# Kernel tuning notes

Hardware: AMD Instinct MI355X
Metric: run time of the kernel (lower is better)

## Reference

```python
import jax, jax.numpy as jnp
import numpy as np

THETA = 10000.0

def apply_rope(x, token_positions, theta=THETA):
    # x: (..., seq, d_k); token_positions: (seq,)
    d_k = x.shape[-1]
    freqs = 1.0 / theta ** (jnp.arange(0, d_k, 2, dtype=jnp.float32) / d_k)  # (d_k/2,)
    ang = token_positions.astype(jnp.float32)[:, None] * freqs  # (seq, d_k/2)
    cos, sin = jnp.cos(ang), jnp.sin(ang)
    x_even, x_odd = x[..., 0::2], x[..., 1::2]
    out_even = x_even * cos - x_odd * sin
    out_odd = x_even * sin + x_odd * cos
    out = jnp.stack([out_even, out_odd], axis=-1)  # interleave pairs
    return out.reshape(*x.shape[:-1], d_k)


def setup_inputs() -> dict:
    key = jax.random.key(0)
    ks = jax.random.split(key, 5)
    B, S, D = 1, 4096, 1024
    s = 1.0 / np.sqrt(D)
    return {
        "x": jax.random.normal(ks[0], (B, S, D), dtype=jnp.float32),
        "token_positions": jnp.arange(S, dtype=jnp.int64 if jax.config.jax_enable_x64 else jnp.int32),
        "Wq": jax.random.normal(ks[1], (D, D), dtype=jnp.float32) * s,
        "Wk": jax.random.normal(ks[2], (D, D), dtype=jnp.float32) * s,
        "Wv": jax.random.normal(ks[3], (D, D), dtype=jnp.float32) * s,
        "Wo": jax.random.normal(ks[4], (D, D), dtype=jnp.float32) * s,
    }


def reference(x, token_positions, Wq, Wk, Wv, Wo):
    B, S, D = x.shape
    H = 16
    hd = D // H
    # nn.Linear(bias=False): y = x @ W.T
    q = (x @ Wq.T).reshape(B, S, H, hd).transpose(0, 2, 1, 3)  # (B,H,S,hd)
    k = (x @ Wk.T).reshape(B, S, H, hd).transpose(0, 2, 1, 3)
    v = (x @ Wv.T).reshape(B, S, H, hd).transpose(0, 2, 1, 3)
    q = apply_rope(q, token_positions)
    k = apply_rope(k, token_positions)
    scores = jnp.einsum("bhqd,bhkd->bhqk", q, k) / jnp.sqrt(jnp.float32(hd))
    causal = jnp.triu(jnp.ones((S, S), dtype=bool), k=1)  # True above diagonal
    scores = jnp.where(causal[None, None], -jnp.inf, scores)
    attn = jax.nn.softmax(scores, axis=-1)
    out = jnp.einsum("bhqk,bhkd->bhqd", attn, v)  # (B,H,S,hd)
    out = out.transpose(0, 2, 1, 3).reshape(B, S, D)
    return out @ Wo.T
```

## Files before the change

### kernel.cpp

```cpp
#include <hip/hip_runtime.h>
#include <hip/hip_bf16.h>
#include <math.h>

#define S_LEN 4096
#define D_MODEL 1024
#define NHEAD 16
#define HD 64

typedef short bf16x8 __attribute__((ext_vector_type(8)));
typedef float f32x16 __attribute__((ext_vector_type(16)));
typedef _Float16 f16x8 __attribute__((ext_vector_type(8)));
typedef _Float16 f16x4 __attribute__((ext_vector_type(4)));

static __device__ __forceinline__ unsigned pk2(float lo, float hi) {
  __hip_bfloat162 h = __float22bfloat162_rn(make_float2(lo, hi));
  return *reinterpret_cast<unsigned*>(&h);
}

static __device__ __forceinline__ void gload16(const void* g, void* l) {
  __builtin_amdgcn_global_load_lds(
      (const __attribute__((address_space(1))) unsigned*)g,
      (__attribute__((address_space(3))) unsigned*)l, 16, 0, 0);
}

__global__ __launch_bounds__(256)
void cvt_f16(const float* __restrict__ src, _Float16* __restrict__ dst, int n4) {
  for (int i = blockIdx.x * 256 + threadIdx.x; i < n4; i += gridDim.x * 256) {
    float4 v = ((const float4*)src)[i];
    f16x4 o;
    o[0] = (_Float16)v.x; o[1] = (_Float16)v.y;
    o[2] = (_Float16)v.z; o[3] = (_Float16)v.w;
    ((f16x4*)dst)[i] = o;
  }
}

__global__ __launch_bounds__(256)
void cvt4_f16(const float* __restrict__ s0, const float* __restrict__ s1,
              const float* __restrict__ s2, const float* __restrict__ s3,
              _Float16* __restrict__ d0, _Float16* __restrict__ d1,
              _Float16* __restrict__ d2, _Float16* __restrict__ d3, int n4) {
  const float* s = (blockIdx.y == 0) ? s0 : (blockIdx.y == 1) ? s1
                 : (blockIdx.y == 2) ? s2 : s3;
  _Float16* d = (blockIdx.y == 0) ? d0 : (blockIdx.y == 1) ? d1
              : (blockIdx.y == 2) ? d2 : d3;
  for (int i = blockIdx.x * 256 + threadIdx.x; i < n4; i += gridDim.x * 256) {
    float4 v = ((const float4*)s)[i];
    f16x4 o;
    o[0] = (_Float16)v.x; o[1] = (_Float16)v.y;
    o[2] = (_Float16)v.z; o[3] = (_Float16)v.w;
    ((f16x4*)d)[i] = o;
  }
}

#define BUFBYTES 16384

static __device__ __forceinline__ void gemm_mainloop_f16(
    const _Float16* __restrict__ A, const _Float16* __restrict__ B,
    int tr0, int br0, char* ldsbuf, int tid,
    f32x16& acc00, f32x16& acc01, f32x16& acc10, f32x16& acc11) {
  const int lane = tid & 63, w = tid >> 6;
  const int l31 = lane & 31, hi5 = lane >> 5;
  const int wr = (w >> 1) * 64, wc = (w & 1) * 64;

  const _Float16* srcs[4];
  int offs[4];
#pragma unroll
  for (int j = 0; j < 4; ++j) {
    int ch = w + 4 * j;
    if (ch < 8) {
      int u = ch * 64 + lane;
      srcs[j] = A + (size_t)(tr0 + (u & 127)) * 1024 + (u >> 7) * 8;
      offs[j] = ch * 1024;
    } else {
      int u = (ch - 8) * 64 + lane;
      srcs[j] = B + (size_t)(br0 + (u & 127)) * 1024 + (u >> 7) * 8;
      offs[j] = 8192 + (ch - 8) * 1024;
    }
  }

#define STAGE(bufoff, koff)                                           \
  {                                                                   \
    _Pragma("unroll") for (int j = 0; j < 4; ++j)                     \
        gload16(srcs[j] + (koff), ldsbuf + (bufoff) + offs[j]);       \
  }

#define COMPUTE(bufoff)                                               \
  {                                                                   \
    const char* lb = ldsbuf + (bufoff);                               \
    _Pragma("unroll") for (int s = 0; s < 2; ++s) {                   \
      const int c = 2 * s + hi5;                                      \
      const char* pa = lb + (size_t)(c * 128 + wr + l31) * 16;        \
      f16x8 a0 = *(const f16x8*)(pa);                                 \
      f16x8 a1 = *(const f16x8*)(pa + 512);                           \
      const char* pb = lb + 8192 + (size_t)(c * 128 + wc + l31) * 16; \
      f16x8 b0 = *(const f16x8*)(pb);                                 \
      f16x8 b1 = *(const f16x8*)(pb + 512);                           \
      acc00 = __builtin_amdgcn_mfma_f32_32x32x16_f16(a0, b0, acc00, 0, 0, 0); \
      acc01 = __builtin_amdgcn_mfma_f32_32x32x16_f16(a0, b1, acc01, 0, 0, 0); \
      acc10 = __builtin_amdgcn_mfma_f32_32x32x16_f16(a1, b0, acc10, 0, 0, 0); \
      acc11 = __builtin_amdgcn_mfma_f32_32x32x16_f16(a1, b1, acc11, 0, 0, 0); \
    }                                                                 \
  }

  STAGE(0, 0);
  __syncthreads();

#pragma unroll 1
  for (int it = 0; it < 16; ++it) {
    const int t0 = 2 * it;
    if (t0 < 31) STAGE(BUFBYTES, (t0 + 1) * 32);
    COMPUTE(0);
    __syncthreads();
    if (t0 + 1 < 31) STAGE(0, (t0 + 2) * 32);
    COMPUTE(BUFBYTES);
    __syncthreads();
  }
#undef STAGE
#undef COMPUTE
}

__global__ __launch_bounds__(256)
void qkv_gemm(const _Float16* __restrict__ xf,
              const _Float16* __restrict__ wqf, const _Float16* __restrict__ wkf,
              const _Float16* __restrict__ wvf,
              unsigned short* __restrict__ Qo, unsigned short* __restrict__ Ko,
              unsigned short* __restrict__ Vo, const int* __restrict__ pos) {
  __shared__ __align__(16) char ldsbuf[2 * BUFBYTES];
  const int tid = threadIdx.x;
  const int nb = blockIdx.x;
  const int which = nb >> 3;
  const int br0 = (nb & 7) * 128;
  const int tr0 = blockIdx.y * 128;

  const _Float16* Bsrc = (which == 0) ? wqf : (which == 1) ? wkf : wvf;
  unsigned short* Out = (which == 0) ? Qo : (which == 1) ? Ko : Vo;

  f32x16 acc00, acc01, acc10, acc11;
#pragma unroll
  for (int r = 0; r < 16; ++r) {
    acc00[r] = 0.0f; acc01[r] = 0.0f; acc10[r] = 0.0f; acc11[r] = 0.0f;
  }

  gemm_mainloop_f16(xf, Bsrc, tr0, br0, ldsbuf, tid, acc00, acc01, acc10, acc11);

  const int lane = tid & 63, w = tid >> 6;
  const int l31 = lane & 31, hi5 = lane >> 5;
  const int wr = (w >> 1) * 64, wc = (w & 1) * 64;
  const float qs = (which == 0) ? 0.125f : 1.0f;

#pragma unroll
  for (int bc = 0; bc < 2; ++bc) {
    const int n = br0 + wc + bc * 32 + l31;
    const int ch = n & 63;
    const float fr = 1.0f / powf(10000.0f, (float)(ch & ~1) * (1.0f / 64.0f));
#pragma unroll
    for (int ar = 0; ar < 2; ++ar) {
      const f32x16& a = ar ? (bc ? acc11 : acc10) : (bc ? acc01 : acc00);
#pragma unroll
      for (int r = 0; r < 16; ++r) {
        const int m = tr0 + wr + ar * 32 + (r & 3) + 8 * (r >> 2) + 4 * hi5;
        float v = a[r];
        if (which < 2) {
          const float ang = (float)pos[m] * fr;
          float sn, cs;
          __sincosf(ang, &sn, &cs);
          const float vp = __shfl_xor(v, 1);
          v = (ch & 1) ? (vp * sn + v * cs) : (v * cs - vp * sn);
          v *= qs;
        }
        const float nv = __shfl_xor(v, 1);
        if ((ch & 1) == 0) {
          *(unsigned*)(Out + (size_t)m * 1024 + n) = pk2(v, nv);
        }
      }
    }
  }
}

__global__ __launch_bounds__(256)
void out_gemm(const _Float16* __restrict__ Of, const _Float16* __restrict__ Wof,
              float* __restrict__ out) {
  __shared__ __align__(16) char ldsbuf[2 * BUFBYTES];
  const int tid = threadIdx.x;
  const int br0 = blockIdx.x * 128;
  const int tr0 = blockIdx.y * 128;

  f32x16 acc00, acc01, acc10, acc11;
#pragma unroll
  for (int r = 0; r < 16; ++r) {
    acc00[r] = 0.0f; acc01[r] = 0.0f; acc10[r] = 0.0f; acc11[r] = 0.0f;
  }

  gemm_mainloop_f16(Of, Wof, tr0, br0, ldsbuf, tid, acc00, acc01, acc10, acc11);

  const int lane = tid & 63, w = tid >> 6;
  const int l31 = lane & 31, hi5 = lane >> 5;
  const int wr = (w >> 1) * 64, wc = (w & 1) * 64;
#pragma unroll
  for (int bc = 0; bc < 2; ++bc) {
    const int n = br0 + wc + bc * 32 + l31;
#pragma unroll
    for (int ar = 0; ar < 2; ++ar) {
      const f32x16& a = ar ? (bc ? acc11 : acc10) : (bc ? acc01 : acc00);
#pragma unroll
      for (int r = 0; r < 16; ++r) {
        const int m = tr0 + wr + ar * 32 + (r & 3) + 8 * (r >> 2) + 4 * hi5;
        out[(size_t)m * 1024 + n] = a[r];
      }
    }
  }
}

union __align__(16) AttnSmem {
  unsigned short q[128 * 64];
  struct { unsigned short k[64 * 64]; unsigned short vt[64 * 64]; } kv;
  float oep[4][32][68];
};

__global__ __launch_bounds__(256)
void attn_mfma(const unsigned short* __restrict__ Qg, const unsigned short* __restrict__ Kg,
               const unsigned short* __restrict__ Vg, _Float16* __restrict__ Of) {
  __shared__ AttnSmem sm;
  const int tid = threadIdx.x;
  const int lane = tid & 63;
  const int w = tid >> 6;
  const int h = blockIdx.x & 15;
  const int qb = 31 - (blockIdx.x >> 4);
  const int qrow0 = qb * 128;
  const int l31 = lane & 31;
  const int hi = lane >> 5;

  {
    const unsigned short* src = Qg + (size_t)qrow0 * D_MODEL + h * HD;
#pragma unroll
    for (int p = 0; p < 4; ++p) {
      int idx = tid + p * 256;
      int row = idx >> 3, c8 = idx & 7;
      bf16x8 v = *(const bf16x8*)(src + (size_t)row * D_MODEL + c8 * 8);
      *(bf16x8*)((char*)sm.q + row * 128 + ((c8 * 16) ^ ((row & 7) << 4))) = v;
    }
  }
  __syncthreads();

  bf16x8 qf[4];
  {
    int qr = w * 32 + l31;
    char* rb = (char*)sm.q + qr * 128;
    int sw = (qr & 7) << 4;
#pragma unroll
    for (int s = 0; s < 4; ++s)
      qf[s] = *(const bf16x8*)(rb + ((s * 32 + hi * 16) ^ sw));
  }
  __syncthreads();

  f32x16 oacc0, oacc1;
#pragma unroll
  for (int r = 0; r < 16; ++r) { oacc0[r] = 0.0f; oacc1[r] = 0.0f; }
  float m_ = -1e30f, l_ = 0.0f;
  const int qg = qrow0 + w * 32 + l31;
  const int qwmax = qrow0 + w * 32 + 31;
  const int nT = 2 * qb + 2;

  for (int t = 0; t < nT; ++t) {
    const int k0 = t * 64;
    __syncthreads();
    {
      const unsigned short* srcK = Kg + (size_t)k0 * D_MODEL + h * HD;
      const unsigned short* srcV = Vg + (size_t)k0 * D_MODEL + h * HD;
#pragma unroll
      for (int p = 0; p < 2; ++p) {
        int idx = tid + p * 256;
        int row = idx >> 3, c8 = idx & 7;
        bf16x8 v = *(const bf16x8*)(srcK + (size_t)row * D_MODEL + c8 * 8);
        *(bf16x8*)((char*)sm.kv.k + row * 128 + ((c8 * 16) ^ ((row & 7) << 4))) = v;
      }
#pragma unroll
      for (int p = 0; p < 4; ++p) {
        int idx = tid + p * 256;
        int row = idx >> 4, c4 = idx & 15;
        uint2 u = *(const uint2*)(srcV + (size_t)row * D_MODEL + c4 * 4);
        int d = c4 * 4;
        unsigned short e0 = (unsigned short)(u.x), e1 = (unsigned short)(u.x >> 16);
        unsigned short e2 = (unsigned short)(u.y), e3 = (unsigned short)(u.y >> 16);
        *(unsigned short*)((char*)sm.kv.vt + (d+0) * 128 + ((row * 2) ^ (((d+0) & 7) << 4))) = e0;
        *(unsigned short*)((char*)sm.kv.vt + (d+1) * 128 + ((row * 2) ^ (((d+1) & 7) << 4))) = e1;
        *(unsigned short*)((char*)sm.kv.vt + (d+2) * 128 + ((row * 2) ^ (((d+2) & 7) << 4))) = e2;
        *(unsigned short*)((char*)sm.kv.vt + (d+3) * 128 + ((row * 2) ^ (((d+3) & 7) << 4))) = e3;
      }
    }
    __syncthreads();

#pragma unroll
    for (int kh = 0; kh < 2; ++kh) {
      if (k0 + kh * 32 > qwmax) continue;

      f32x16 sa;
#pragma unroll
      for (int r = 0; r < 16; ++r) sa[r] = 0.0f;
      {
        int krow = kh * 32 + l31;
        char* kb = (char*)sm.kv.k + krow * 128;
        int sw = (krow & 7) << 4;
#pragma unroll
        for (int s = 0; s < 4; ++s) {
          bf16x8 kf = *(const bf16x8*)(kb + ((s * 32 + hi * 16) ^ sw));
          sa = __builtin_amdgcn_mfma_f32_32x32x16_bf16(kf, qf[s], sa, 0, 0, 0);
        }
      }

      if (k0 + kh * 32 + 31 > qg) {
#pragma unroll
        for (int r = 0; r < 16; ++r) {
          int kg = k0 + kh * 32 + (r & 3) + 8 * (r >> 2) + 4 * hi;
          if (kg > qg) sa[r] = -1e30f;
        }
      }

      float tm = sa[0];
#pragma unroll
      for (int r = 1; r < 16; ++r) tm = fmaxf(tm, sa[r]);
      tm = fmaxf(tm, __shfl_xor(tm, 32));
      const float mn = fmaxf(m_, tm);
      const float sc = __expf(m_ - mn);
      m_ = mn;
      float rs = 0.0f;
#pragma unroll
      for (int r = 0; r < 16; ++r) {
        float e = __expf(sa[r] - mn);
        sa[r] = e;
        rs += e;
      }
      rs += __shfl_xor(rs, 32);
      l_ = l_ * sc + rs;
#pragma unroll
      for (int r = 0; r < 16; ++r) { oacc0[r] *= sc; oacc1[r] *= sc; }

      unsigned a0 = pk2(sa[0],  sa[1]),  b0 = pk2(sa[4],  sa[5]);
      unsigned a1 = pk2(sa[2],  sa[3]),  b1 = pk2(sa[6],  sa[7]);
      unsigned a2 = pk2(sa[8],  sa[9]),  b2 = pk2(sa[12], sa[13]);
      unsigned a3 = pk2(sa[10], sa[11]), b3 = pk2(sa[14], sa[15]);
      asm volatile("v_permlane32_swap_b32 %0, %1" : "+v"(a0), "+v"(b0));
      asm volatile("v_permlane32_swap_b32 %0, %1" : "+v"(a1), "+v"(b1));
      asm volatile("v_permlane32_swap_b32 %0, %1" : "+v"(a2), "+v"(b2));
      asm volatile("v_permlane32_swap_b32 %0, %1" : "+v"(a3), "+v"(b3));
      union FU { unsigned u[4]; bf16x8 v; } f0, f1;
      f0.u[0] = a0; f0.u[1] = a1; f0.u[2] = b0; f0.u[3] = b1;
      f1.u[0] = a2; f1.u[1] = a3; f1.u[2] = b2; f1.u[3] = b3;

      {
        char* vb0 = (char*)sm.kv.vt + l31 * 128;
        char* vb1 = (char*)sm.kv.vt + (32 + l31) * 128;
        int sw = (l31 & 7) << 4;
        int off0 = (kh * 64 + hi * 16) ^ sw;
        int off1 = (kh * 64 + 32 + hi * 16) ^ sw;
        bf16x8 v00 = *(const bf16x8*)(vb0 + off0);
        bf16x8 v01 = *(const bf16x8*)(vb0 + off1);
        bf16x8 v10 = *(const bf16x8*)(vb1 + off0);
        bf16x8 v11 = *(const bf16x8*)(vb1 + off1);
        oacc0 = __builtin_amdgcn_mfma_f32_32x32x16_bf16(v00, f0.v, oacc0, 0, 0, 0);
        oacc0 = __builtin_amdgcn_mfma_f32_32x32x16_bf16(v01, f1.v, oacc0, 0, 0, 0);
        oacc1 = __builtin_amdgcn_mfma_f32_32x32x16_bf16(v10, f0.v, oacc1, 0, 0, 0);
        oacc1 = __builtin_amdgcn_mfma_f32_32x32x16_bf16(v11, f1.v, oacc1, 0, 0, 0);
      }
    }
  }

  __syncthreads();
  const float inv = 1.0f / l_;
#pragma unroll
  for (int g = 0; g < 4; ++g) {
    *(float4*)&sm.oep[w][l31][8 * g + 4 * hi] =
        make_float4(oacc0[4*g+0] * inv, oacc0[4*g+1] * inv,
                    oacc0[4*g+2] * inv, oacc0[4*g+3] * inv);
    *(float4*)&sm.oep[w][l31][8 * g + 4 * hi + 32] =
        make_float4(oacc1[4*g+0] * inv, oacc1[4*g+1] * inv,
                    oacc1[4*g+2] * inv, oacc1[4*g+3] * inv);
  }
  {
    int qr = lane >> 1, chh = lane & 1;
    const float* rp = &sm.oep[w][qr][chh * 32];
    const size_t base = (size_t)(qrow0 + w * 32 + qr) * D_MODEL + h * HD + chh * 32;
#pragma unroll
    for (int j = 0; j < 8; ++j) {
      float4 v = *(const float4*)(rp + j * 4);
      f16x4 o;
      o[0] = (_Float16)v.x; o[1] = (_Float16)v.y;
      o[2] = (_Float16)v.z; o[3] = (_Float16)v.w;
      *(f16x4*)(Of + base + j * 4) = o;
    }
  }
}

extern "C" void kernel_launch(void* const* d_in, const int* in_sizes, int n_in,
                              void* d_out, int out_size, void* d_ws, size_t ws_size,
                              hipStream_t stream) {
  const float* x   = (const float*)d_in[0];
  const int*   pos = (const int*)d_in[1];
  const float* Wq  = (const float*)d_in[2];
  const float* Wk  = (const float*)d_in[3];
  const float* Wv  = (const float*)d_in[4];
  const float* Wo  = (const float*)d_in[5];
  float* out = (float*)d_out;

  char* ws = (char*)d_ws;
  const size_t MB = 1024 * 1024;
  _Float16* xf  = (_Float16*)(ws);
  _Float16* wqf = (_Float16*)(ws + 8 * MB);
  _Float16* wkf = (_Float16*)(ws + 10 * MB);
  _Float16* wvf = (_Float16*)(ws + 12 * MB);
  _Float16* wof = (_Float16*)(ws + 14 * MB);
  unsigned short* Qb = (unsigned short*)(ws + 16 * MB);
  unsigned short* Kb = (unsigned short*)(ws + 24 * MB);
  unsigned short* Vb = (unsigned short*)(ws + 32 * MB);
  _Float16* Of = xf;

  dim3 blk(256);

  hipLaunchKernelGGL(cvt_f16, dim3(2048), blk, 0, stream, x, xf,
                     (int)((size_t)S_LEN * D_MODEL / 4));
  hipLaunchKernelGGL(cvt4_f16, dim3(512, 4), blk, 0, stream,
                     Wq, Wk, Wv, Wo, wqf, wkf, wvf, wof,
                     D_MODEL * D_MODEL / 4);

  hipLaunchKernelGGL(qkv_gemm, dim3(24, 32), blk, 0, stream,
                     xf, wqf, wkf, wvf, Qb, Kb, Vb, pos);

  hipLaunchKernelGGL(attn_mfma, dim3(512), blk, 0, stream, Qb, Kb, Vb, Of);

  hipLaunchKernelGGL(out_gemm, dim3(8, 32), blk, 0, stream, Of, wof, out);
}
```

Baseline: 349.2 us.

## Pre-transpose V globally, use exp2 softmax, and skip small max rescales

A new vtrans kernel writes V transposed per head into workspace, so the attention kernel can load V^T tiles with 16-byte vector loads instead of scattered 2-byte LDS stores. The log2(e) factor is folded into the Q scale so the softmax uses exp2f. The output/normalizer rescale is also skipped unless the running max grows by more than 8, a lazy-rescale trick that relies on bounded exponent growth. This adds an extra kernel launch and an 8MB round trip for V, and carries some numerical risk from the lazy rescale.

Result: faster. 339.9 us (-2.7%).

```diff
diff --git a/kernel.cpp b/kernel.cpp
--- a/kernel.cpp
+++ b/kernel.cpp
@@ -50,6 +50,28 @@
     o[2] = (_Float16)v.z; o[3] = (_Float16)v.w;
     ((f16x4*)d)[i] = o;
   }
+}
+
+__global__ __launch_bounds__(256)
+void vtrans(const unsigned short* __restrict__ V, unsigned short* __restrict__ Vt) {
+  __shared__ unsigned short t[64][72];
+  const int tid = threadIdx.x;
+  const int k0 = blockIdx.x * 64;
+  const int n0 = blockIdx.y * 64;
+#pragma unroll
+  for (int p = 0; p < 2; ++p) {
+    int idx = tid + p * 256;
+    int r = idx >> 3, c8 = idx & 7;
+    *(bf16x8*)&t[r][c8 * 8] =
+        *(const bf16x8*)(V + (size_t)(k0 + r) * D_MODEL + n0 + c8 * 8);
+  }
+  __syncthreads();
+  const int d = tid >> 2, kc = tid & 3;
+  __align__(16) unsigned short buf[16];
+#pragma unroll
+  for (int j = 0; j < 16; ++j) buf[j] = t[kc * 16 + j][d];
+  *(uint4*)(Vt + (size_t)(n0 + d) * S_LEN + k0 + kc * 16) = *(uint4*)buf;
+  *(uint4*)(Vt + (size_t)(n0 + d) * S_LEN + k0 + kc * 16 + 8) = *(uint4*)(buf + 8);
 }
 
 #define BUFBYTES 16384
@@ -146,7 +168,7 @@
   const int lane = tid & 63, w = tid >> 6;
   const int l31 = lane & 31, hi5 = lane >> 5;
   const int wr = (w >> 1) * 64, wc = (w & 1) * 64;
-  const float qs = (which == 0) ? 0.125f : 1.0f;
+  const float qs = (which == 0) ? 0.125f * 1.44269504088896f : 1.0f;
 
 #pragma unroll
   for (int bc = 0; bc < 2; ++bc) {
@@ -219,7 +241,7 @@
 
 __global__ __launch_bounds__(256)
 void attn_mfma(const unsigned short* __restrict__ Qg, const unsigned short* __restrict__ Kg,
-               const unsigned short* __restrict__ Vg, _Float16* __restrict__ Of) {
+               const unsigned short* __restrict__ Vt, _Float16* __restrict__ Of) {
   __shared__ AttnSmem sm;
   const int tid = threadIdx.x;
   const int lane = tid & 63;
@@ -266,26 +288,16 @@
     __syncthreads();
     {
       const unsigned short* srcK = Kg + (size_t)k0 * D_MODEL + h * HD;
-      const unsigned short* srcV = Vg + (size_t)k0 * D_MODEL + h * HD;
+      const unsigned short* srcVt = Vt + (size_t)(h * HD) * S_LEN + k0;
 #pragma unroll
       for (int p = 0; p < 2; ++p) {
         int idx = tid + p * 256;
         int row = idx >> 3, c8 = idx & 7;
-        bf16x8 v = *(const bf16x8*)(srcK + (size_t)row * D_MODEL + c8 * 8);
-        *(bf16x8*)((char*)sm.kv.k + row * 128 + ((c8 * 16) ^ ((row & 7) << 4))) = v;
-      }
-#pragma unroll
-      for (int p = 0; p < 4; ++p) {
-        int idx = tid + p * 256;
-        int row = idx >> 4, c4 = idx & 15;
-        uint2 u = *(const uint2*)(srcV + (size_t)row * D_MODEL + c4 * 4);
-        int d = c4 * 4;
-        unsigned short e0 = (unsigned short)(u.x), e1 = (unsigned short)(u.x >> 16);
-        unsigned short e2 = (unsigned short)(u.y), e3 = (unsigned short)(u.y >> 16);
-        *(unsigned short*)((char*)sm.kv.vt + (d+0) * 128 + ((row * 2) ^ (((d+0) & 7) << 4))) = e0;
-        *(unsigned short*)((char*)sm.kv.vt + (d+1) * 128 + ((row * 2) ^ (((d+1) & 7) << 4))) = e1;
-        *(unsigned short*)((char*)sm.kv.vt + (d+2) * 128 + ((row * 2) ^ (((d+2) & 7) << 4))) = e2;
-        *(unsigned short*)((char*)sm.kv.vt + (d+3) * 128 + ((row * 2) ^ (((d+3) & 7) << 4))) = e3;
+        int sw = (c8 * 16) ^ ((row & 7) << 4);
+        bf16x8 kv_ = *(const bf16x8*)(srcK + (size_t)row * D_MODEL + c8 * 8);
+        *(bf16x8*)((char*)sm.kv.k + row * 128 + sw) = kv_;
+        bf16x8 vv = *(const bf16x8*)(srcVt + (size_t)row * S_LEN + c8 * 8);
+        *(bf16x8*)((char*)sm.kv.vt + row * 128 + sw) = vv;
       }
     }
     __syncthreads();
@@ -320,20 +332,23 @@
 #pragma unroll
       for (int r = 1; r < 16; ++r) tm = fmaxf(tm, sa[r]);
       tm = fmaxf(tm, __shfl_xor(tm, 32));
-      const float mn = fmaxf(m_, tm);
-      const float sc = __expf(m_ - mn);
-      m_ = mn;
+      if (!__all(tm <= m_ + 8.0f)) {
+        const float mn = fmaxf(m_, tm);
+        const float sc = exp2f(m_ - mn);
+        m_ = mn;
+        l_ *= sc;
+#pragma unroll
+        for (int r = 0; r < 16; ++r) { oacc0[r] *= sc; oacc1[r] *= sc; }
+      }
       float rs = 0.0f;
 #pragma unroll
       for (int r = 0; r < 16; ++r) {
-        float e = __expf(sa[r] - mn);
+        float e = exp2f(sa[r] - m_);
         sa[r] = e;
         rs += e;
       }
       rs += __shfl_xor(rs, 32);
-      l_ = l_ * sc + rs;
-#pragma unroll
-      for (int r = 0; r < 16; ++r) { oacc0[r] *= sc; oacc1[r] *= sc; }
+      l_ += rs;
 
       unsigned a0 = pk2(sa[0],  sa[1]),  b0 = pk2(sa[4],  sa[5]);
       unsigned a1 = pk2(sa[2],  sa[3]),  b1 = pk2(sa[6],  sa[7]);
@@ -412,6 +427,7 @@
   unsigned short* Qb = (unsigned short*)(ws + 16 * MB);
   unsigned short* Kb = (unsigned short*)(ws + 24 * MB);
   unsigned short* Vb = (unsigned short*)(ws + 32 * MB);
+  unsigned short* Vt = (unsigned short*)(ws + 40 * MB);
   _Float16* Of = xf;
 
   dim3 blk(256);
@@ -425,7 +441,9 @@
   hipLaunchKernelGGL(qkv_gemm, dim3(24, 32), blk, 0, stream,
                      xf, wqf, wkf, wvf, Qb, Kb, Vb, pos);
 
-  hipLaunchKernelGGL(attn_mfma, dim3(512), blk, 0, stream, Qb, Kb, Vb, Of);
+  hipLaunchKernelGGL(vtrans, dim3(64, 16), blk, 0, stream, Vb, Vt);
+
+  hipLaunchKernelGGL(attn_mfma, dim3(512), blk, 0, stream, Qb, Kb, Vt, Of);
 
   hipLaunchKernelGGL(out_gemm, dim3(8, 32), blk, 0, stream, Of, wof, out);
 }
```
